# Kernel tuning notes

Measured on AMD Instinct MI355X. Metric: run time of the kernel, lower is better.

The kernel has to match this reference:

```python
import jax, jax.numpy as jnp
import numpy as np

T = 1_000_000  # total packed nodes
B = 4096       # number of graphs
NC = 7         # num_classes (EC top-level classes)
EPS = 1e-5


def _bn(h, p):
    # p: [4, C] stacked (gamma, beta, running_mean, running_var); eval-mode BatchNorm
    g, b, m, v = p[0], p[1], p[2], p[3]
    return (h - m) * jax.lax.rsqrt(v + EPS) * g + b


def setup_inputs() -> dict:
    key = jax.random.key(0)
    ks = jax.random.split(key, 32)

    def w(k, shape, s=0.1):
        return (jax.random.normal(k, shape, dtype=jnp.float32) * s)

    def bn(k, c):
        return jnp.stack([
            jnp.ones((c,), jnp.float32),                         # gamma
            jnp.zeros((c,), jnp.float32),                        # beta
            jax.random.normal(k, (c,), dtype=jnp.float32) * 0.1, # running mean
            jax.random.uniform(k, (c,), jnp.float32, 0.5, 1.5),  # running var
        ])

    inp = {
        "x": jax.random.normal(ks[0], (T,), dtype=jnp.float32),
        "batch": jnp.sort(jax.random.randint(ks[1], (T,), 0, B, dtype=jnp.int32)),
        "num_graphs": B,
        # node_embedding: Linear(1,32)+ReLU+BN1d(32)+Linear(32,64)+ReLU+BN1d(64)
        "ne_w1": w(ks[2], (1, 32)), "ne_b1": w(ks[3], (32,)), "ne_bn1": bn(ks[4], 32),
        "ne_w2": w(ks[5], (32, 64)), "ne_b2": w(ks[6], (64,)), "ne_bn2": bn(ks[7], 64),
        # MLPBlock([64,64,64]) = two 1x1 convs + ReLU, then BatchNorm2d(64)
        "c1a_w": w(ks[8], (64, 64)), "c1a_b": w(ks[9], (64,)),
        "c1b_w": w(ks[10], (64, 64)), "c1b_b": w(ks[11], (64,)), "cbn1": bn(ks[12], 64),
        # MLPBlock([64,128,128]) then BatchNorm2d(128)
        "c2a_w": w(ks[13], (64, 128)), "c2a_b": w(ks[14], (128,)),
        "c2b_w": w(ks[15], (128, 128)), "c2b_b": w(ks[16], (128,)), "cbn2": bn(ks[17], 128),
        # final_mlp: 128->64 (BN) -> 64->32 (BN) -> 32->7 ; Dropout is identity in eval
        "f1_w": w(ks[18], (128, 64)), "f1_b": w(ks[19], (64,)), "fbn1": bn(ks[20], 64),
        "f2_w": w(ks[21], (64, 32)), "f2_b": w(ks[22], (32,)), "fbn2": bn(ks[23], 32),
        "f3_w": w(ks[24], (32, NC)), "f3_b": w(ks[25], (NC,)),
    }
    return inp


def reference(x, batch, num_graphs,
              ne_w1, ne_b1, ne_bn1, ne_w2, ne_b2, ne_bn2,
              c1a_w, c1a_b, c1b_w, c1b_b, cbn1,
              c2a_w, c2a_b, c2b_w, c2b_b, cbn2,
              f1_w, f1_b, fbn1, f2_w, f2_b, fbn2, f3_w, f3_b):
    # node embedding over packed nodes [T] -> [T,64]
    h = x[:, None]
    h = _bn(jax.nn.relu(h @ ne_w1 + ne_b1), ne_bn1)
    h = _bn(jax.nn.relu(h @ ne_w2 + ne_b2), ne_bn2)
    # conv blocks are 1x1 (input is [1,C,N,1]) => pointwise per node; BN2d eval-mode
    h = jax.nn.relu(h @ c1a_w + c1a_b)
    h = jax.nn.relu(h @ c1b_w + c1b_b)
    h = _bn(h, cbn1)
    h = jax.nn.relu(h @ c2a_w + c2a_b)
    h = jax.nn.relu(h @ c2b_w + c2b_b)
    h = _bn(h, cbn2)                                     # [T,128]
    # mean over nodes of each graph (the per-graph loop's .mean(dim=2))
    sums = jax.ops.segment_sum(h, batch, num_segments=num_graphs)           # [B,128]
    cnts = jax.ops.segment_sum(jnp.ones((h.shape[0],), h.dtype), batch,
                               num_segments=num_graphs)
    g = sums / jnp.maximum(cnts, 1.0)[:, None]
    # final mlp (Dropout = identity in eval)
    g = _bn(jax.nn.relu(g @ f1_w + f1_b), fbn1)
    g = _bn(jax.nn.relu(g @ f2_w + f2_b), fbn2)
    return g @ f3_w + f3_b                                # [B, NC]
```

## Files before the change

kernel.cpp:

```cpp
#include <hip/hip_runtime.h>
#include <math.h>


#define EPSBN 1e-5f
#define SPW 4
#define TILE 1024

template <int CIN, int COUT, bool RELU, bool BN>
__device__ __forceinline__ void dense_stage(const float (*in)[SPW], float (*out)[SPW],
                                            const float* __restrict__ W,
                                            const float* __restrict__ bias,
                                            const float* __restrict__ bs,
                                            const float* __restrict__ bt, int lane)
{
    float acc0[SPW], acc1[SPW];
    const float b0 = bias[lane];
    const float b1 = (COUT == 128) ? bias[lane + 64] : 0.f;
#pragma unroll
    for (int i = 0; i < SPW; i++) { acc0[i] = b0; acc1[i] = b1; }
    for (int k = 0; k < CIN; k++) {
        const float4 h = *(const float4*)&in[k][0];
        const float hv[4] = {h.x, h.y, h.z, h.w};
        const float w0 = W[k * COUT + lane];
        const float w1 = (COUT == 128) ? W[k * COUT + lane + 64] : 0.f;
#pragma unroll
        for (int i = 0; i < SPW; i++) {
            acc0[i] = fmaf(hv[i], w0, acc0[i]);
            if (COUT == 128) acc1[i] = fmaf(hv[i], w1, acc1[i]);
        }
    }
    const float s0 = BN ? bs[lane] : 1.f;
    const float t0 = BN ? bt[lane] : 0.f;
    const float s1 = (BN && COUT == 128) ? bs[lane + 64] : 1.f;
    const float t1 = (BN && COUT == 128) ? bt[lane + 64] : 0.f;
#pragma unroll
    for (int i = 0; i < SPW; i++) {
        float r0 = RELU ? fmaxf(acc0[i], 0.f) : acc0[i];
        out[lane][i] = BN ? fmaf(s0, r0, t0) : r0;
        if (COUT == 128) {
            float r1 = RELU ? fmaxf(acc1[i], 0.f) : acc1[i];
            out[lane + 64][i] = BN ? fmaf(s1, r1, t1) : r1;
        }
    }
}

__global__ __launch_bounds__(256) void table_kernel(
    const float* __restrict__ ne_w1, const float* __restrict__ ne_b1,
    const float* __restrict__ ne_w2, const float* __restrict__ ne_b2,
    const float* __restrict__ ne_bn1, const float* __restrict__ ne_bn2,
    const float* __restrict__ c1a_w, const float* __restrict__ c1a_b,
    const float* __restrict__ c1b_w, const float* __restrict__ c1b_b,
    const float* __restrict__ cbn1,
    const float* __restrict__ c2a_w, const float* __restrict__ c2a_b,
    const float* __restrict__ c2b_w, const float* __restrict__ c2b_b,
    const float* __restrict__ cbn2,
    const float* __restrict__ f1_w,
    float* __restrict__ table2, float* __restrict__ zero_base, int zero_n,
    float xmin, float dx)
{
    __shared__ __align__(16) float bufA[4][128][SPW];
    __shared__ __align__(16) float bufB[4][128][SPW];
    __shared__ float s1v[32], t1v[32], s2v[64], t2v[64];
    __shared__ float s3v[64], t3v[64], s4v[128], t4v[128];

    const int tid = threadIdx.x;

    {
        const int gtid = blockIdx.x * 256 + tid;
        const int gstride = gridDim.x * 256;
        for (int idx = gtid; idx < zero_n; idx += gstride) zero_base[idx] = 0.f;
    }

    for (int cc = tid; cc < 288; cc += 256) {
        int c = cc;
        const float* bn; float* ps; float* pt; int C;
        if (c < 32)       { bn = ne_bn1; ps = s1v; pt = t1v; C = 32; }
        else if (c < 96)  { c -= 32;  bn = ne_bn2; ps = s2v; pt = t2v; C = 64; }
        else if (c < 160) { c -= 96;  bn = cbn1;   ps = s3v; pt = t3v; C = 64; }
        else              { c -= 160; bn = cbn2;   ps = s4v; pt = t4v; C = 128; }
        float s = bn[c] * rsqrtf(bn[3 * C + c] + EPSBN);
        ps[c] = s;
        pt[c] = bn[C + c] - bn[2 * C + c] * s;
    }
    __syncthreads();

    const int wv = tid >> 6;
    const int lane = tid & 63;
    const int s0i = (blockIdx.x * 4 + wv) * SPW;

    float xs[SPW];
#pragma unroll
    for (int i = 0; i < SPW; i++) xs[i] = xmin + dx * (float)(s0i + i);

    {
        float acc[SPW];
        const float b = ne_b2[lane];
#pragma unroll
        for (int i = 0; i < SPW; i++) acc[i] = b;
        for (int k = 0; k < 32; k++) {
            const float w = ne_w2[k * 64 + lane];
            const float a1 = ne_w1[k], c1 = ne_b1[k];
            const float sk = s1v[k], tk = t1v[k];
#pragma unroll
            for (int i = 0; i < SPW; i++) {
                float h1 = fmaxf(fmaf(xs[i], a1, c1), 0.f);
                acc[i] = fmaf(fmaf(sk, h1, tk), w, acc[i]);
            }
        }
        const float s2l = s2v[lane], t2l = t2v[lane];
#pragma unroll
        for (int i = 0; i < SPW; i++)
            bufA[wv][lane][i] = fmaf(s2l, fmaxf(acc[i], 0.f), t2l);
    }
    __syncthreads();
    dense_stage<64, 64, true, false>(bufA[wv], bufB[wv], c1a_w, c1a_b, nullptr, nullptr, lane);
    __syncthreads();
    dense_stage<64, 64, true, true>(bufB[wv], bufA[wv], c1b_w, c1b_b, s3v, t3v, lane);
    __syncthreads();
    dense_stage<64, 128, true, false>(bufA[wv], bufB[wv], c2a_w, c2a_b, nullptr, nullptr, lane);
    __syncthreads();
    dense_stage<128, 128, true, true>(bufB[wv], bufA[wv], c2b_w, c2b_b, s4v, t4v, lane);
    __syncthreads();
    {
        float acc[SPW] = {0.f, 0.f, 0.f, 0.f};
        for (int k = 0; k < 128; k++) {
            const float4 h = *(const float4*)&bufA[wv][k][0];
            const float w = f1_w[k * 64 + lane];
            acc[0] = fmaf(h.x, w, acc[0]);
            acc[1] = fmaf(h.y, w, acc[1]);
            acc[2] = fmaf(h.z, w, acc[2]);
            acc[3] = fmaf(h.w, w, acc[3]);
        }
#pragma unroll
        for (int i = 0; i < SPW; i++) {
            const int s = s0i + i;
            table2[((size_t)s * 64 + lane) * 2] = acc[i];
            if (s > 0) table2[((size_t)(s - 1) * 64 + lane) * 2 + 1] = acc[i];
        }
    }
}

__global__ __launch_bounds__(256) void node_kernel(
    const float* __restrict__ x, const int* __restrict__ batch,
    const float* __restrict__ table2, float* __restrict__ zsum,
    float* __restrict__ cnt,
    int T, int mtab, float xmin, float inv_dx)
{
    __shared__ __align__(16) int sg[TILE];
    __shared__ __align__(16) int si[TILE];
    __shared__ __align__(16) float sa[TILE];
    const int tid = threadIdx.x;
    const int base = blockIdx.x * TILE;
    const float2* __restrict__ tab2 = (const float2*)table2;

    for (int idx = tid; idx < TILE; idx += 256) {
        int t = base + idx;
        int g = -1, i = 0;
        float a = 0.f;
        if (t < T) {
            g = batch[t];
            float f = (x[t] - xmin) * inv_dx;
            f = fminf(fmaxf(f, 0.f), (float)(mtab - 1) - 0.001f);
            i = (int)f;
            a = f - (float)i;
        }
        sg[idx] = g;
        si[idx] = i;
        sa[idx] = a;
    }
    __syncthreads();

    const int wv = tid >> 6, lane = tid & 63;
    int cur_g = -1;
    int run = 0;
    float acc = 0.f;
    for (int j4 = 0; j4 < 256 / 4; ++j4) {
        const int idx0 = wv * 256 + j4 * 4;
        const int4 g4 = *(const int4*)&sg[idx0];
        const int4 i4 = *(const int4*)&si[idx0];
        const float4 a4 = *(const float4*)&sa[idx0];
        float2 w0 = tab2[(size_t)i4.x * 64 + lane];
        float2 w1 = tab2[(size_t)i4.y * 64 + lane];
        float2 w2 = tab2[(size_t)i4.z * 64 + lane];
        float2 w3 = tab2[(size_t)i4.w * 64 + lane];
        const int gs[4] = {g4.x, g4.y, g4.z, g4.w};
        const float as[4] = {a4.x, a4.y, a4.z, a4.w};
        const float2 ws[4] = {w0, w1, w2, w3};
#pragma unroll
        for (int n = 0; n < 4; n++) {
            float val = fmaf(as[n], ws[n].y - ws[n].x, ws[n].x);
            if (gs[n] != cur_g) {
                if (cur_g >= 0) {
                    atomicAdd(&zsum[(size_t)cur_g * 64 + lane], acc);
                    if (lane == 0) atomicAdd(&cnt[cur_g], (float)run);
                }
                cur_g = gs[n];
                acc = val;
                run = 1;
            } else {
                acc += val;
                run++;
            }
        }
    }
    if (cur_g >= 0) {
        atomicAdd(&zsum[(size_t)cur_g * 64 + lane], acc);
        if (lane == 0) atomicAdd(&cnt[cur_g], (float)run);
    }
}

__global__ __launch_bounds__(256) void head_kernel(
    const float* __restrict__ zsum, const float* __restrict__ cnt, int B,
    const float* __restrict__ f1_b, const float* __restrict__ fbn1,
    const float* __restrict__ f2_w, const float* __restrict__ f2_b,
    const float* __restrict__ fbn2,
    const float* __restrict__ f3_w, const float* __restrict__ f3_b,
    float* __restrict__ out)
{
    __shared__ float ld[256 * 65];
    __shared__ float s5[64], t5[64], s6[32], t6[32];
    const int tid = threadIdx.x;
    if (tid < 96) {
        int c = tid;
        const float* bn; float* ps; float* pt; int C;
        if (c < 64) { bn = fbn1; ps = s5; pt = t5; C = 64; }
        else        { c -= 64; bn = fbn2; ps = s6; pt = t6; C = 32; }
        float s = bn[c] * rsqrtf(bn[3 * C + c] + EPSBN);
        ps[c] = s;
        pt[c] = bn[C + c] - bn[2 * C + c] * s;
    }

    const int gbase = blockIdx.x * 256;
    for (int idx = tid; idx < 256 * 64; idx += 256) {
        const int gidx = gbase * 64 + idx;
        float v = (gidx < B * 64) ? zsum[gidx] : 0.f;
        const int r = idx >> 6, c = idx & 63;
        ld[r * 65 + c] = v;
    }
    __syncthreads();

    const int g = gbase + tid;
    if (g >= B) return;
    const float cN = cnt[g];
    const float inv = (cN > 0.5f) ? 1.0f / cN : 1.0f;
    const float* zs = &ld[tid * 65];

    float g1[64];
#pragma unroll
    for (int j = 0; j < 64; j++) {
        float v = fmaxf(fmaf(zs[j], inv, f1_b[j]), 0.f);
        g1[j] = fmaf(s5[j], v, t5[j]);
    }

    float g2[32];
    for (int jj = 0; jj < 32; jj++) {
        float acc = f2_b[jj];
#pragma unroll
        for (int j = 0; j < 64; j++) acc = fmaf(g1[j], f2_w[j * 32 + jj], acc);
        float v = fmaxf(acc, 0.f);
        g2[jj] = fmaf(s6[jj], v, t6[jj]);
    }
    for (int o = 0; o < 7; o++) {
        float acc = f3_b[o];
#pragma unroll
        for (int jj = 0; jj < 32; jj++) acc = fmaf(g2[jj], f3_w[jj * 7 + o], acc);
        out[(size_t)g * 7 + o] = acc;
    }
}

extern "C" void kernel_launch(void* const* d_in, const int* in_sizes, int n_in,
                              void* d_out, int out_size, void* d_ws, size_t ws_size,
                              hipStream_t stream)
{
    const float* x      = (const float*)d_in[0];
    const int*   batch  = (const int*)d_in[1];
    const float* ne_w1  = (const float*)d_in[3];
    const float* ne_b1  = (const float*)d_in[4];
    const float* ne_bn1 = (const float*)d_in[5];
    const float* ne_w2  = (const float*)d_in[6];
    const float* ne_b2  = (const float*)d_in[7];
    const float* ne_bn2 = (const float*)d_in[8];
    const float* c1a_w  = (const float*)d_in[9];
    const float* c1a_b  = (const float*)d_in[10];
    const float* c1b_w  = (const float*)d_in[11];
    const float* c1b_b  = (const float*)d_in[12];
    const float* cbn1   = (const float*)d_in[13];
    const float* c2a_w  = (const float*)d_in[14];
    const float* c2a_b  = (const float*)d_in[15];
    const float* c2b_w  = (const float*)d_in[16];
    const float* c2b_b  = (const float*)d_in[17];
    const float* cbn2   = (const float*)d_in[18];
    const float* f1_w   = (const float*)d_in[19];
    const float* f1_b   = (const float*)d_in[20];
    const float* fbn1   = (const float*)d_in[21];
    const float* f2_w   = (const float*)d_in[22];
    const float* f2_b   = (const float*)d_in[23];
    const float* fbn2   = (const float*)d_in[24];
    const float* f3_w   = (const float*)d_in[25];
    const float* f3_b   = (const float*)d_in[26];

    const int T = in_sizes[0];
    const int B = out_size / 7;
    float* wsf = (float*)d_ws;

    int M = 4096;
    while (M > 512 && (size_t)((size_t)M * 128 + (size_t)B * 65) * 4 > ws_size) M >>= 1;
    const float xmin = -6.5f;
    const float dx = 13.0f / (float)M;
    const float inv_dx = (float)M / 13.0f;

    float* table2 = wsf;
    float* zsum = table2 + (size_t)M * 128;
    float* cnt = zsum + (size_t)B * 64;
    const int zero_n = B * 65;

    table_kernel<<<M / 16, 256, 0, stream>>>(ne_w1, ne_b1, ne_w2, ne_b2, ne_bn1, ne_bn2,
                                             c1a_w, c1a_b, c1b_w, c1b_b, cbn1,
                                             c2a_w, c2a_b, c2b_w, c2b_b, cbn2,
                                             f1_w, table2, zsum, zero_n, xmin, dx);
    node_kernel<<<(T + TILE - 1) / TILE, 256, 0, stream>>>(x, batch, table2, zsum, cnt,
                                                           T, M, xmin, inv_dx);
    head_kernel<<<(B + 255) / 256, 256, 0, stream>>>(zsum, cnt, B, f1_b,
                                                     fbn1, f2_w, f2_b, fbn2, f3_w, f3_b,
                                                     (float*)d_out);
}
```

Before: 204.0 us.

## Fuse table, node and head kernels into one persistent kernel with grid barriers

Merges the three launches into one persistent kernel of 256 blocks that builds the lookup table, crosses a software grid barrier, runs the node gather and segment accumulation in a grid-stride tile loop, crosses a second barrier, and then runs the per-graph head MLP. The aim is to remove launch gaps and inter-kernel drain between the three stages. In exchange it adds an atomic-spin grid barrier that depends on all 256 blocks being co-resident, plus a memset for the barrier counters. The head stage now runs on only one thread in sixteen with 16 graphs per block, which lowers parallelism in that stage, and the table size is fixed at 4096 with no check against workspace size.

```diff
diff --git a/kernel.cpp b/kernel.cpp
--- a/kernel.cpp
+++ b/kernel.cpp
@@ -5,6 +5,8 @@
 #define EPSBN 1e-5f
 #define SPW 4
 #define TILE 1024
+#define NB 256
+#define M_TAB 4096
 
 template <int CIN, int COUT, bool RELU, bool BN>
 __device__ __forceinline__ void dense_stage(const float (*in)[SPW], float (*out)[SPW],
@@ -44,7 +46,20 @@
     }
 }
 
-__global__ __launch_bounds__(256) void table_kernel(
+__device__ __forceinline__ void grid_barrier(unsigned* ctr)
+{
+    __syncthreads();
+    if (threadIdx.x == 0) {
+        __threadfence();
+        atomicAdd(ctr, 1u);
+        while (atomicAdd(ctr, 0u) < (unsigned)NB) __builtin_amdgcn_s_sleep(2);
+    }
+    __syncthreads();
+    __threadfence();
+}
+
+__global__ __launch_bounds__(256) void fused_kernel(
+    const float* __restrict__ x, const int* __restrict__ batch, int T, int B,
     const float* __restrict__ ne_w1, const float* __restrict__ ne_b1,
     const float* __restrict__ ne_w2, const float* __restrict__ ne_b2,
     const float* __restrict__ ne_bn1, const float* __restrict__ ne_bn2,
@@ -54,21 +69,32 @@
     const float* __restrict__ c2a_w, const float* __restrict__ c2a_b,
     const float* __restrict__ c2b_w, const float* __restrict__ c2b_b,
     const float* __restrict__ cbn2,
-    const float* __restrict__ f1_w,
-    float* __restrict__ table2, float* __restrict__ zero_base, int zero_n,
-    float xmin, float dx)
+    const float* __restrict__ f1_w, const float* __restrict__ f1_b,
+    const float* __restrict__ fbn1,
+    const float* __restrict__ f2_w, const float* __restrict__ f2_b,
+    const float* __restrict__ fbn2,
+    const float* __restrict__ f3_w, const float* __restrict__ f3_b,
+    float* __restrict__ table2, float* __restrict__ zsum, float* __restrict__ cnt,
+    unsigned* __restrict__ bar,
+    float* __restrict__ out, float xmin, float dx, float inv_dx)
 {
     __shared__ __align__(16) float bufA[4][128][SPW];
     __shared__ __align__(16) float bufB[4][128][SPW];
+    __shared__ __align__(16) int sg[TILE];
+    __shared__ __align__(16) int si[TILE];
+    __shared__ __align__(16) float sa[TILE];
     __shared__ float s1v[32], t1v[32], s2v[64], t2v[64];
     __shared__ float s3v[64], t3v[64], s4v[128], t4v[128];
+    __shared__ float s5[64], t5[64], s6[32], t6[32];
 
     const int tid = threadIdx.x;
+    const int wv = tid >> 6;
+    const int lane = tid & 63;
 
     {
+        const int zero_n = B * 65;
         const int gtid = blockIdx.x * 256 + tid;
-        const int gstride = gridDim.x * 256;
-        for (int idx = gtid; idx < zero_n; idx += gstride) zero_base[idx] = 0.f;
+        for (int idx = gtid; idx < zero_n; idx += NB * 256) zsum[idx] = 0.f;
     }
 
     for (int cc = tid; cc < 288; cc += 256) {
@@ -84,142 +110,125 @@
     }
     __syncthreads();
 
-    const int wv = tid >> 6;
-    const int lane = tid & 63;
-    const int s0i = (blockIdx.x * 4 + wv) * SPW;
-
-    float xs[SPW];
-#pragma unroll
-    for (int i = 0; i < SPW; i++) xs[i] = xmin + dx * (float)(s0i + i);
-
     {
-        float acc[SPW];
-        const float b = ne_b2[lane];
-#pragma unroll
-        for (int i = 0; i < SPW; i++) acc[i] = b;
-        for (int k = 0; k < 32; k++) {
-            const float w = ne_w2[k * 64 + lane];
-            const float a1 = ne_w1[k], c1 = ne_b1[k];
-            const float sk = s1v[k], tk = t1v[k];
+        const int s0i = (blockIdx.x * 4 + wv) * SPW;
+        float xs[SPW];
+#pragma unroll
+        for (int i = 0; i < SPW; i++) xs[i] = xmin + dx * (float)(s0i + i);
+
+        {
+            float acc[SPW];
+            const float b = ne_b2[lane];
+#pragma unroll
+            for (int i = 0; i < SPW; i++) acc[i] = b;
+            for (int k = 0; k < 32; k++) {
+                const float w = ne_w2[k * 64 + lane];
+                const float a1 = ne_w1[k], c1 = ne_b1[k];
+                const float sk = s1v[k], tk = t1v[k];
+#pragma unroll
+                for (int i = 0; i < SPW; i++) {
+                    float h1 = fmaxf(fmaf(xs[i], a1, c1), 0.f);
+                    acc[i] = fmaf(fmaf(sk, h1, tk), w, acc[i]);
+                }
+            }
+            const float s2l = s2v[lane], t2l = t2v[lane];
+#pragma unroll
+            for (int i = 0; i < SPW; i++)
+                bufA[wv][lane][i] = fmaf(s2l, fmaxf(acc[i], 0.f), t2l);
+        }
+        __syncthreads();
+        dense_stage<64, 64, true, false>(bufA[wv], bufB[wv], c1a_w, c1a_b, nullptr, nullptr, lane);
+        __syncthreads();
+        dense_stage<64, 64, true, true>(bufB[wv], bufA[wv], c1b_w, c1b_b, s3v, t3v, lane);
+        __syncthreads();
+        dense_stage<64, 128, true, false>(bufA[wv], bufB[wv], c2a_w, c2a_b, nullptr, nullptr, lane);
+        __syncthreads();
+        dense_stage<128, 128, true, true>(bufB[wv], bufA[wv], c2b_w, c2b_b, s4v, t4v, lane);
+        __syncthreads();
+        {
+            float acc[SPW] = {0.f, 0.f, 0.f, 0.f};
+            for (int k = 0; k < 128; k++) {
+                const float4 h = *(const float4*)&bufA[wv][k][0];
+                const float w = f1_w[k * 64 + lane];
+                acc[0] = fmaf(h.x, w, acc[0]);
+                acc[1] = fmaf(h.y, w, acc[1]);
+                acc[2] = fmaf(h.z, w, acc[2]);
+                acc[3] = fmaf(h.w, w, acc[3]);
+            }
 #pragma unroll
             for (int i = 0; i < SPW; i++) {
-                float h1 = fmaxf(fmaf(xs[i], a1, c1), 0.f);
-                acc[i] = fmaf(fmaf(sk, h1, tk), w, acc[i]);
-            }
-        }
-        const float s2l = s2v[lane], t2l = t2v[lane];
-#pragma unroll
-        for (int i = 0; i < SPW; i++)
-            bufA[wv][lane][i] = fmaf(s2l, fmaxf(acc[i], 0.f), t2l);
-    }
-    __syncthreads();
-    dense_stage<64, 64, true, false>(bufA[wv], bufB[wv], c1a_w, c1a_b, nullptr, nullptr, lane);
-    __syncthreads();
-    dense_stage<64, 64, true, true>(bufB[wv], bufA[wv], c1b_w, c1b_b, s3v, t3v, lane);
-    __syncthreads();
-    dense_stage<64, 128, true, false>(bufA[wv], bufB[wv], c2a_w, c2a_b, nullptr, nullptr, lane);
-    __syncthreads();
-    dense_stage<128, 128, true, true>(bufB[wv], bufA[wv], c2b_w, c2b_b, s4v, t4v, lane);
-    __syncthreads();
+                const int s = s0i + i;
+                table2[((size_t)s * 64 + lane) * 2] = acc[i];
+                if (s > 0) table2[((size_t)(s - 1) * 64 + lane) * 2 + 1] = acc[i];
+            }
+        }
+    }
+
+    grid_barrier(&bar[0]);
+
     {
-        float acc[SPW] = {0.f, 0.f, 0.f, 0.f};
-        for (int k = 0; k < 128; k++) {
-            const float4 h = *(const float4*)&bufA[wv][k][0];
-            const float w = f1_w[k * 64 + lane];
-            acc[0] = fmaf(h.x, w, acc[0]);
-            acc[1] = fmaf(h.y, w, acc[1]);
-            acc[2] = fmaf(h.z, w, acc[2]);
-            acc[3] = fmaf(h.w, w, acc[3]);
-        }
-#pragma unroll
-        for (int i = 0; i < SPW; i++) {
-            const int s = s0i + i;
-            table2[((size_t)s * 64 + lane) * 2] = acc[i];
-            if (s > 0) table2[((size_t)(s - 1) * 64 + lane) * 2 + 1] = acc[i];
-        }
-    }
-}
-
-__global__ __launch_bounds__(256) void node_kernel(
-    const float* __restrict__ x, const int* __restrict__ batch,
-    const float* __restrict__ table2, float* __restrict__ zsum,
-    float* __restrict__ cnt,
-    int T, int mtab, float xmin, float inv_dx)
-{
-    __shared__ __align__(16) int sg[TILE];
-    __shared__ __align__(16) int si[TILE];
-    __shared__ __align__(16) float sa[TILE];
-    const int tid = threadIdx.x;
-    const int base = blockIdx.x * TILE;
-    const float2* __restrict__ tab2 = (const float2*)table2;
-
-    for (int idx = tid; idx < TILE; idx += 256) {
-        int t = base + idx;
-        int g = -1, i = 0;
-        float a = 0.f;
-        if (t < T) {
-            g = batch[t];
-            float f = (x[t] - xmin) * inv_dx;
-            f = fminf(fmaxf(f, 0.f), (float)(mtab - 1) - 0.001f);
-            i = (int)f;
-            a = f - (float)i;
-        }
-        sg[idx] = g;
-        si[idx] = i;
-        sa[idx] = a;
-    }
-    __syncthreads();
-
-    const int wv = tid >> 6, lane = tid & 63;
-    int cur_g = -1;
-    int run = 0;
-    float acc = 0.f;
-    for (int j4 = 0; j4 < 256 / 4; ++j4) {
-        const int idx0 = wv * 256 + j4 * 4;
-        const int4 g4 = *(const int4*)&sg[idx0];
-        const int4 i4 = *(const int4*)&si[idx0];
-        const float4 a4 = *(const float4*)&sa[idx0];
-        float2 w0 = tab2[(size_t)i4.x * 64 + lane];
-        float2 w1 = tab2[(size_t)i4.y * 64 + lane];
-        float2 w2 = tab2[(size_t)i4.z * 64 + lane];
-        float2 w3 = tab2[(size_t)i4.w * 64 + lane];
-        const int gs[4] = {g4.x, g4.y, g4.z, g4.w};
-        const float as[4] = {a4.x, a4.y, a4.z, a4.w};
-        const float2 ws[4] = {w0, w1, w2, w3};
-#pragma unroll
-        for (int n = 0; n < 4; n++) {
-            float val = fmaf(as[n], ws[n].y - ws[n].x, ws[n].x);
-            if (gs[n] != cur_g) {
-                if (cur_g >= 0) {
-                    atomicAdd(&zsum[(size_t)cur_g * 64 + lane], acc);
-                    if (lane == 0) atomicAdd(&cnt[cur_g], (float)run);
+        const float2* __restrict__ tab2 = (const float2*)table2;
+        const int ntiles = (T + TILE - 1) / TILE;
+        for (int tile = blockIdx.x; tile < ntiles; tile += NB) {
+            const int base = tile * TILE;
+            for (int idx = tid; idx < TILE; idx += 256) {
+                int t = base + idx;
+                int g = -1, i = 0;
+                float a = 0.f;
+                if (t < T) {
+                    g = batch[t];
+                    float f = (x[t] - xmin) * inv_dx;
+                    f = fminf(fmaxf(f, 0.f), (float)(M_TAB - 1) - 0.001f);
+                    i = (int)f;
+                    a = f - (float)i;
                 }
-                cur_g = gs[n];
-                acc = val;
-                run = 1;
-            } else {
-                acc += val;
-                run++;
-            }
-        }
-    }
-    if (cur_g >= 0) {
-        atomicAdd(&zsum[(size_t)cur_g * 64 + lane], acc);
-        if (lane == 0) atomicAdd(&cnt[cur_g], (float)run);
-    }
-}
-
-__global__ __launch_bounds__(256) void head_kernel(
-    const float* __restrict__ zsum, const float* __restrict__ cnt, int B,
-    const float* __restrict__ f1_b, const float* __restrict__ fbn1,
-    const float* __restrict__ f2_w, const float* __restrict__ f2_b,
-    const float* __restrict__ fbn2,
-    const float* __restrict__ f3_w, const float* __restrict__ f3_b,
-    float* __restrict__ out)
-{
-    __shared__ float ld[256 * 65];
-    __shared__ float s5[64], t5[64], s6[32], t6[32];
-    const int tid = threadIdx.x;
+                sg[idx] = g;
+                si[idx] = i;
+                sa[idx] = a;
+            }
+            __syncthreads();
+
+            int cur_g = -1, run = 0;
+            float acc = 0.f;
+            for (int j4 = 0; j4 < 256 / 4; ++j4) {
+                const int idx0 = wv * 256 + j4 * 4;
+                const int4 g4 = *(const int4*)&sg[idx0];
+                const int4 i4 = *(const int4*)&si[idx0];
+                const float4 a4 = *(const float4*)&sa[idx0];
+                const float2 w0 = tab2[(size_t)i4.x * 64 + lane];
+                const float2 w1 = tab2[(size_t)i4.y * 64 + lane];
+                const float2 w2 = tab2[(size_t)i4.z * 64 + lane];
+                const float2 w3 = tab2[(size_t)i4.w * 64 + lane];
+                const int gs[4] = {g4.x, g4.y, g4.z, g4.w};
+                const float as[4] = {a4.x, a4.y, a4.z, a4.w};
+                const float2 ws[4] = {w0, w1, w2, w3};
+#pragma unroll
+                for (int n = 0; n < 4; n++) {
+                    float val = fmaf(as[n], ws[n].y - ws[n].x, ws[n].x);
+                    if (gs[n] != cur_g) {
+                        if (cur_g >= 0) {
+                            atomicAdd(&zsum[(size_t)cur_g * 64 + lane], acc);
+                            if (lane == 0) atomicAdd(&cnt[cur_g], (float)run);
+                        }
+                        cur_g = gs[n];
+                        acc = val;
+                        run = 1;
+                    } else {
+                        acc += val;
+                        run++;
+                    }
+                }
+            }
+            if (cur_g >= 0) {
+                atomicAdd(&zsum[(size_t)cur_g * 64 + lane], acc);
+                if (lane == 0) atomicAdd(&cnt[cur_g], (float)run);
+            }
+            __syncthreads();
+        }
+    }
+
+    grid_barrier(&bar[16]);
+
     if (tid < 96) {
         int c = tid;
         const float* bn; float* ps; float* pt; int C;
@@ -229,42 +238,42 @@
         ps[c] = s;
         pt[c] = bn[C + c] - bn[2 * C + c] * s;
     }
-
-    const int gbase = blockIdx.x * 256;
-    for (int idx = tid; idx < 256 * 64; idx += 256) {
-        const int gidx = gbase * 64 + idx;
-        float v = (gidx < B * 64) ? zsum[gidx] : 0.f;
-        const int r = idx >> 6, c = idx & 63;
-        ld[r * 65 + c] = v;
-    }
     __syncthreads();
 
-    const int g = gbase + tid;
-    if (g >= B) return;
-    const float cN = cnt[g];
-    const float inv = (cN > 0.5f) ? 1.0f / cN : 1.0f;
-    const float* zs = &ld[tid * 65];
-
-    float g1[64];
-#pragma unroll
-    for (int j = 0; j < 64; j++) {
-        float v = fmaxf(fmaf(zs[j], inv, f1_b[j]), 0.f);
-        g1[j] = fmaf(s5[j], v, t5[j]);
-    }
-
-    float g2[32];
-    for (int jj = 0; jj < 32; jj++) {
-        float acc = f2_b[jj];
-#pragma unroll
-        for (int j = 0; j < 64; j++) acc = fmaf(g1[j], f2_w[j * 32 + jj], acc);
-        float v = fmaxf(acc, 0.f);
-        g2[jj] = fmaf(s6[jj], v, t6[jj]);
-    }
-    for (int o = 0; o < 7; o++) {
-        float acc = f3_b[o];
-#pragma unroll
-        for (int jj = 0; jj < 32; jj++) acc = fmaf(g2[jj], f3_w[jj * 7 + o], acc);
-        out[(size_t)g * 7 + o] = acc;
+    if ((tid & 15) == 0) {
+        const int g = blockIdx.x * 16 + (tid >> 4);
+        if (g < B) {
+            const float cN = cnt[g];
+            const float inv = (cN > 0.5f) ? 1.0f / cN : 1.0f;
+            const float4* z4 = (const float4*)(zsum + (size_t)g * 64);
+
+            float g1[64];
+#pragma unroll
+            for (int jq = 0; jq < 16; jq++) {
+                const float4 z = z4[jq];
+                const float zz[4] = {z.x, z.y, z.z, z.w};
+#pragma unroll
+                for (int u = 0; u < 4; u++) {
+                    const int j = jq * 4 + u;
+                    float v = fmaxf(fmaf(zz[u], inv, f1_b[j]), 0.f);
+                    g1[j] = fmaf(s5[j], v, t5[j]);
+                }
+            }
+            float g2[32];
+            for (int jj = 0; jj < 32; jj++) {
+                float acc = f2_b[jj];
+#pragma unroll
+                for (int j = 0; j < 64; j++) acc = fmaf(g1[j], f2_w[j * 32 + jj], acc);
+                float v = fmaxf(acc, 0.f);
+                g2[jj] = fmaf(s6[jj], v, t6[jj]);
+            }
+            for (int o = 0; o < 7; o++) {
+                float acc = f3_b[o];
+#pragma unroll
+                for (int jj = 0; jj < 32; jj++) acc = fmaf(g2[jj], f3_w[jj * 7 + o], acc);
+                out[(size_t)g * 7 + o] = acc;
+            }
+        }
     }
 }
 
@@ -301,26 +310,24 @@
 
     const int T = in_sizes[0];
     const int B = out_size / 7;
+
+    const float xmin = -6.5f;
+    const float dx = 13.0f / (float)M_TAB;
+    const float inv_dx = (float)M_TAB / 13.0f;
+
     float* wsf = (float*)d_ws;
-
-    int M = 4096;
-    while (M > 512 && (size_t)((size_t)M * 128 + (size_t)B * 65) * 4 > ws_size) M >>= 1;
-    const float xmin = -6.5f;
-    const float dx = 13.0f / (float)M;
-    const float inv_dx = (float)M / 13.0f;
-
     float* table2 = wsf;
-    float* zsum = table2 + (size_t)M * 128;
+    float* zsum = table2 + (size_t)M_TAB * 128;
     float* cnt = zsum + (size_t)B * 64;
-    const int zero_n = B * 65;
-
-    table_kernel<<<M / 16, 256, 0, stream>>>(ne_w1, ne_b1, ne_w2, ne_b2, ne_bn1, ne_bn2,
-                                             c1a_w, c1a_b, c1b_w, c1b_b, cbn1,
-                                             c2a_w, c2a_b, c2b_w, c2b_b, cbn2,
-                                             f1_w, table2, zsum, zero_n, xmin, dx);
-    node_kernel<<<(T + TILE - 1) / TILE, 256, 0, stream>>>(x, batch, table2, zsum, cnt,
-                                                           T, M, xmin, inv_dx);
-    head_kernel<<<(B + 255) / 256, 256, 0, stream>>>(zsum, cnt, B, f1_b,
-                                                     fbn1, f2_w, f2_b, fbn2, f3_w, f3_b,
-                                                     (float*)d_out);
+    unsigned* bar = (unsigned*)(cnt + B + 32);
+
+    hipMemsetAsync(bar, 0, 128, stream);
+    fused_kernel<<<NB, 256, 0, stream>>>(x, batch, T, B,
+                                         ne_w1, ne_b1, ne_w2, ne_b2, ne_bn1, ne_bn2,
+                                         c1a_w, c1a_b, c1b_w, c1b_b, cbn1,
+                                         c2a_w, c2a_b, c2b_w, c2b_b, cbn2,
+                                         f1_w, f1_b, fbn1, f2_w, f2_b, fbn2,
+                                         f3_w, f3_b,
+                                         table2, zsum, cnt, bar,
+                                         (float*)d_out, xmin, dx, inv_dx);
 }
```

Measured after the change: 317.0 us. 1.55x slower.
